# Kernel optimization log

Hardware: AMD Instinct MI355X
Metric: run time of the kernel (lower is better)

## Reference

```python
import jax, jax.numpy as jnp
import numpy as np
import math

B, T, D = 4, 2048, 1024
N, D_OUT = 1024, 1024
EPS_A = 1e-4
PROJ_BOUND = 1.0


def setup_inputs() -> dict:
    key = jax.random.key(0)
    ks = jax.random.split(key, 4)
    # reset_parameters: rho=0.99, delta0=1.0
    rho, delta0 = 0.99, 1.0
    alpha0 = -math.log(rho) / delta0
    alpha_log_val = math.log(math.expm1(alpha0))
    delta_bias_val = math.log(math.expm1(delta0))
    return {
        "u": jax.random.normal(ks[0], (B, T, D), dtype=jnp.float32),
        "z0": jnp.zeros((B, N), dtype=jnp.float32),
        "W_in_raw": 0.02 * jax.random.normal(ks[1], (N, D), dtype=jnp.float32),
        "W_out_raw": 0.02 * jax.random.normal(ks[2], (D_OUT, N), dtype=jnp.float32),
        "pn_w": 0.02 * jax.random.normal(ks[3], (3 * N, D), dtype=jnp.float32),
        "pn_b": jnp.zeros((3 * N,), dtype=jnp.float32),
        "alpha_log": jnp.full((N,), alpha_log_val, dtype=jnp.float32),
        "delta_bias": jnp.full((N,), delta_bias_val, dtype=jnp.float32),
        "log_gamma": jnp.float32(0.0),
    }


def _bounded_linear(x, W, bound):
    # y = x @ (W/scale)^T with ||W/scale||_2 <= bound (exact spectral norm)
    sigma = jnp.maximum(jnp.linalg.norm(W, ord=2), 1e-5)
    scale = jnp.maximum(sigma / bound, 1.0)
    return x @ (W / scale).T


def reference(u, z0, W_in_raw, W_out_raw, pn_w, pn_b, alpha_log, delta_bias, log_gamma):
    g = jnp.exp(log_gamma)
    u_scaled = g * _bounded_linear(u, W_in_raw, PROJ_BOUND)        # (B,T,N)
    raw = u @ pn_w.T + pn_b                                        # (B,T,3N)
    delta_raw, b_raw, c_raw = jnp.split(raw, 3, axis=-1)
    delta = jax.nn.softplus(delta_raw + delta_bias)
    alpha = jax.nn.softplus(alpha_log)                             # (N,)
    a = jnp.minimum(jnp.exp(-delta * alpha), 1.0 - EPS_A)          # (B,T,N)
    b = jnp.tanh(b_raw)
    c = jnp.tanh(c_raw)
    # exact spectral norm of [[a,b],[c,0]] per coordinate
    p = a * a + c * c
    r = b * b
    q = a * b
    disc = (p - r) * (p - r) + 4.0 * q * q
    lam_max = 0.5 * (p + r + jnp.sqrt(disc + 1e-12))
    sigma = jnp.sqrt(lam_max + 1e-12)
    scale = jnp.maximum(sigma, 1.0)
    a, b, c = a / scale, b / scale, c / scale
    # diagonal recurrence z_{t+1} = a_t * z_t + b_t * u_scaled_t via associative scan
    bu = b * u_scaled
    bu = bu.at[:, 0].add(a[:, 0] * z0)
    def combine(x, y):
        a1, b1 = x
        a2, b2 = y
        return (a2 * a1, a2 * b1 + b2)
    _, z_next = jax.lax.associative_scan(combine, (a, bu), axis=1)  # z_1..z_T (B,T,N)
    # y_t = W_out (c_t * z_t) with z_t = state BEFORE update (one-step delay)
    states = jnp.concatenate([z0[:, None, :], z_next[:, :-1, :]], axis=1)  # z_0..z_{T-1}
    y_hat = c * states
    y = _bounded_linear(y_hat, W_out_raw, PROJ_BOUND)              # (B,T,D_out)
    return y
```

## Files before the change

kernel.cpp:

```cpp
#include <hip/hip_runtime.h>
#include <stdint.h>

#define B_ 4
#define T_ 2048
#define D_ 1024
#define N_ 1024
#define TC 16
#define NCH (T_/TC)
#define SQN 6

typedef __attribute__((ext_vector_type(4))) float f32x4;
typedef __attribute__((ext_vector_type(8))) short bf16x8;
typedef __attribute__((ext_vector_type(4))) unsigned short us4;

__device__ __forceinline__ unsigned short f2bf(float f){
  unsigned int u = __float_as_uint(f);
  return (unsigned short)((u + 0x7fffu + ((u >> 16) & 1u)) >> 16);
}
__device__ __forceinline__ float bf2f(unsigned short h){
  return __uint_as_float(((unsigned int)h) << 16);
}

__device__ __forceinline__ float inv_scale(const float* __restrict__ sc, int z){
  float ll = 0.f, w = 1.f, t = 1.f;
  #pragma unroll
  for (int i = 0; i <= SQN; i++){
    t = sc[8 + 2*i + z];
    ll += w * __logf(t);
    w *= 0.5f;
  }
  float F = sc[8 + 2*(SQN+1) + z];
  ll += w * __logf(F / (t*t));
  float sig = fmaxf(__expf(0.5f * ll), 1e-5f);
  return 1.f / fmaxf(sig, 1.f);
}

#define U4    2097152
#define WIN4   262144
#define PNW4   786432
#define WOUT4  262144
#define CONV_BLOCKS ((U4 + WIN4 + PNW4 + WOUT4 + 255)/256)

__global__ void k_convert_all(const float* __restrict__ u, const float* __restrict__ Win,
                              const float* __restrict__ pnw, const float* __restrict__ Wout,
                              unsigned short* __restrict__ u16, unsigned short* __restrict__ Wcat16,
                              unsigned short* __restrict__ Wout16, float* __restrict__ sc){
  if (blockIdx.x == 0 && threadIdx.x < 64) sc[threadIdx.x] = 0.f;
  long i = (long)blockIdx.x * 256 + threadIdx.x;
  const float* src; unsigned short* dst; long o;
  if (i < U4)                      { src = u;    dst = u16;               o = i; }
  else if (i < U4+WIN4)            { src = Win;  dst = Wcat16;            o = i - U4; }
  else if (i < U4+WIN4+PNW4)       { src = pnw;  dst = Wcat16 + 1048576;  o = i - (U4+WIN4); }
  else if (i < U4+WIN4+PNW4+WOUT4) { src = Wout; dst = Wout16;            o = i - (U4+WIN4+PNW4); }
  else return;
  float4 v = ((const float4*)src)[o];
  us4 w;
  w.x = f2bf(v.x); w.y = f2bf(v.y); w.z = f2bf(v.z); w.w = f2bf(v.w);
  ((us4*)dst)[o] = w;
}

__device__ __forceinline__ void load_lds16(const unsigned short* g, unsigned short* l){
  __builtin_amdgcn_global_load_lds((const __attribute__((address_space(1))) void*)g,
                                   (__attribute__((address_space(3))) void*)l, 16, 0, 0);
}

template<int OUTBF16>
__global__ __launch_bounds__(256) void k_gemm(
    const unsigned short* __restrict__ A,
    const unsigned short* __restrict__ Bmat,
    void* __restrict__ C0,
    int M, int N, int K,
    const float* __restrict__ sc, int step)
{
  __shared__ alignas(16) unsigned short As[128*64];
  __shared__ alignas(16) unsigned short Bs[128*64];
  const int tid = threadIdx.x;
  const int wid = tid >> 6;
  const int lane = tid & 63;
  const int bn = blockIdx.x, bm = blockIdx.y;

  char* C = (char*)C0;
  float outscale = (step >= 0) ? inv_scale(sc, step) : 1.f;

  const int wr = wid >> 1, wc = wid & 1;
  const int rg = lane >> 3;
  const int cby = (lane & 7) << 4;
  const int srow0 = wid * 32;
  const int frow = lane & 15;
  const int kgrp = lane >> 4;

  const size_t Abase = (size_t)bm * 128 * K;
  const size_t Bbase = (size_t)bn * 128 * K;

  f32x4 acc[4][4] = {};

  for (int kt = 0; kt < K; kt += 64){
    #pragma unroll
    for (int i = 0; i < 4; i++){
      int r = srow0 + i*8 + rg;
      int cb = cby ^ ((r & 7) << 4);
      load_lds16(A    + Abase + (size_t)r*K + kt + (cb >> 1), As + (srow0 + i*8)*64);
      load_lds16(Bmat + Bbase + (size_t)r*K + kt + (cb >> 1), Bs + (srow0 + i*8)*64);
    }
    __syncthreads();
    #pragma unroll
    for (int kk = 0; kk < 2; kk++){
      const int kbyte = kk*64 + kgrp*16;
      bf16x8 af[4], bfv[4];
      #pragma unroll
      for (int m = 0; m < 4; m++){
        int r = wr*64 + m*16 + frow;
        af[m] = *(const bf16x8*)((const char*)As + r*128 + (kbyte ^ ((r & 7) << 4)));
      }
      #pragma unroll
      for (int n2 = 0; n2 < 4; n2++){
        int r = wc*64 + n2*16 + frow;
        bfv[n2] = *(const bf16x8*)((const char*)Bs + r*128 + (kbyte ^ ((r & 7) << 4)));
      }
      #pragma unroll
      for (int m = 0; m < 4; m++)
        #pragma unroll
        for (int n2 = 0; n2 < 4; n2++)
          acc[m][n2] = __builtin_amdgcn_mfma_f32_16x16x32_bf16(af[m], bfv[n2], acc[m][n2], 0, 0, 0);
    }
    __syncthreads();
  }

  const int row0 = bm*128 + wr*64;
  const int col0 = bn*128 + wc*64 + frow;
  #pragma unroll
  for (int m = 0; m < 4; m++){
    #pragma unroll
    for (int n2 = 0; n2 < 4; n2++){
      const int col = col0 + n2*16;
      const int rb = row0 + m*16 + kgrp*4;
      #pragma unroll
      for (int j = 0; j < 4; j++){
        float v = acc[m][n2][j] * outscale;
        if (OUTBF16) ((unsigned short*)C)[(size_t)(rb + j)*N + col] = f2bf(v);
        else         ((float*)C)[(size_t)(rb + j)*N + col] = v;
      }
    }
  }
}

__global__ __launch_bounds__(256) void k_sq(
    const unsigned short* __restrict__ A0, unsigned short* __restrict__ C0,
    const unsigned short* __restrict__ A1, unsigned short* __restrict__ C1,
    float* __restrict__ sc, int step)
{
  __shared__ alignas(16) unsigned short As0[64*128], Bs0[64*128];
  __shared__ alignas(16) unsigned short As1[64*128], Bs1[64*128];
  const int tid = threadIdx.x;
  const int wid = tid >> 6;
  const int lane = tid & 63;
  const int z = blockIdx.z;

  int x = blockIdx.x, bm = 0;
  while (x >= 16 - bm){ x -= 16 - bm; bm++; }
  const int bn = bm + x;

  const unsigned short* A = z ? A1 : A0;
  unsigned short* C = z ? C1 : C0;
  float outscale = 1.f;
  if (step > 0){ float t = sc[8 + (step-1)*2 + z]; outscale = 1.f/(t*t); }

  const int wr = wid >> 1, wc = wid & 1;
  const int frow = lane & 15;
  const int kgrp = lane >> 4;

  const int srl = lane >> 4;
  const int sgr = lane & 15;
  const int swzr = wid*4 + srl;
  const int scol_e = ((sgr ^ swzr) << 3);

  const size_t Arow = (size_t)bm * 64;
  const size_t Brow = (size_t)bn * 64;

  f32x4 acc[2][2] = {};

  auto stage = [&](unsigned short* as, unsigned short* bs, int t){
    const int kt = t * 128;
    #pragma unroll
    for (int i = 0; i < 4; i++){
      int r = i*16 + wid*4 + srl;
      load_lds16(A + (Arow + r)*1024 + kt + scol_e, as + (i*16 + wid*4)*128);
      load_lds16(A + (Brow + r)*1024 + kt + scol_e, bs + (i*16 + wid*4)*128);
    }
  };

  auto compute = [&](const unsigned short* as, const unsigned short* bs){
    #pragma unroll
    for (int ks = 0; ks < 4; ks++){
      const int kb = ks*64 + kgrp*16;
      bf16x8 af[2], bfv[2];
      #pragma unroll
      for (int m = 0; m < 2; m++){
        int r = wr*32 + m*16 + frow;
        af[m] = *(const bf16x8*)((const char*)as + r*256 + (kb ^ (frow << 4)));
      }
      #pragma unroll
      for (int n2 = 0; n2 < 2; n2++){
        int r = wc*32 + n2*16 + frow;
        bfv[n2] = *(const bf16x8*)((const char*)bs + r*256 + (kb ^ (frow << 4)));
      }
      #pragma unroll
      for (int m = 0; m < 2; m++)
        #pragma unroll
        for (int n2 = 0; n2 < 2; n2++)
          acc[m][n2] = __builtin_amdgcn_mfma_f32_16x16x32_bf16(af[m], bfv[n2], acc[m][n2], 0, 0, 0);
    }
  };

  stage(As0, Bs0, 0);
  __syncthreads();
  for (int t2 = 0; t2 < 8; t2 += 2){
    if (t2 + 1 < 8) stage(As1, Bs1, t2 + 1);
    compute(As0, Bs0);
    __syncthreads();
    if (t2 + 2 < 8) stage(As0, Bs0, t2 + 2);
    compute(As1, Bs1);
    __syncthreads();
  }

  const int row0 = bm*64 + wr*32;
  const int col0 = bn*64 + wc*32 + frow;
  float fr = 0.f;
  #pragma unroll
  for (int m = 0; m < 2; m++){
    #pragma unroll
    for (int n2 = 0; n2 < 2; n2++){
      const int col = col0 + n2*16;
      const int rb = row0 + m*16 + kgrp*4;
      us4 tw;
      #pragma unroll
      for (int j = 0; j < 4; j++){
        float v = acc[m][n2][j] * outscale;
        unsigned short h = f2bf(v);
        C[(size_t)(rb + j)*1024 + col] = h;
        tw[j] = h;
        fr += v*v;
      }
      if (bm != bn)
        *(us4*)(C + (size_t)col*1024 + rb) = tw;
    }
  }
  if (bm == bn && wr == wc){
    int j = frow - kgrp*4;
    if (j >= 0 && j < 4){
      float d = (acc[0][0][j] + acc[1][1][j]) * outscale;
      atomicAdd(&sc[8 + step*2 + z], d);
    }
  }
  if (step == SQN){
    if (bm != bn) fr *= 2.f;
    #pragma unroll
    for (int off = 32; off; off >>= 1) fr += __shfl_down(fr, off, 64);
    if (lane == 0) atomicAdd(&sc[8 + 2*(SQN+1) + z], fr);
  }
}

__device__ __forceinline__ float softplusf(float x){
  return (x > 0.f) ? (x + __logf(1.f + __expf(-x))) : __logf(1.f + __expf(x));
}
__device__ __forceinline__ float tanhfastf(float x){
  float e = __expf(2.f * x);
  return 1.f - 2.f/(e + 1.f);
}
__device__ __forceinline__ void abc_from(float pin, float draw, float braw, float craw,
    float alpha, float ginv, float& a_o, float& bu_o, float& c_o){
  float sp = softplusf(draw);
  float av = __expf(-sp * alpha);
  av = fminf(av, 1.f - 1e-4f);
  float bv = tanhfastf(braw);
  float cv = tanhfastf(craw);
  float p = av*av + cv*cv;
  float r = bv*bv;
  float q = av*bv;
  float pr = p - r;
  float disc = pr*pr + 4.f*q*q;
  float lam = 0.5f*(p + r + sqrtf(disc + 1e-12f));
  float sig = sqrtf(lam + 1e-12f);
  float inv = 1.f / fmaxf(sig, 1.f);
  a_o = av * inv;
  c_o = cv * inv;
  bu_o = (bv * inv) * (pin * ginv);
}

__global__ __launch_bounds__(256) void k_pass1(
    const unsigned short* __restrict__ P,
    const float* __restrict__ alog, const float* __restrict__ dbias,
    const float* __restrict__ pnb, const float* __restrict__ lgam,
    const float* __restrict__ sc,
    float* __restrict__ Asum, float* __restrict__ Ssum)
{
  const int tid = threadIdx.x;
  const int n0 = tid*4;
  const int ch = blockIdx.x, b = blockIdx.y;
  const float ginv = __expf(lgam[0]) * inv_scale(sc, 0);
  float alpha[4], bd[4], bb[4], bc[4], A[4], S[4];
  #pragma unroll
  for (int j = 0; j < 4; j++){
    alpha[j] = softplusf(alog[n0+j]);
    bd[j] = dbias[n0+j] + pnb[n0+j];
    bb[j] = pnb[N_ + n0+j];
    bc[j] = pnb[2*N_ + n0+j];
    A[j] = 1.f; S[j] = 0.f;
  }
  const unsigned short* Pr = P + (size_t)(b*T_ + ch*TC) * (4*N_);
  #pragma unroll 2
  for (int i = 0; i < TC; i++){
    us4 vp = *(const us4*)(Pr + n0);
    us4 vd = *(const us4*)(Pr + N_ + n0);
    us4 vb = *(const us4*)(Pr + 2*N_ + n0);
    us4 vc = *(const us4*)(Pr + 3*N_ + n0);
    #pragma unroll
    for (int j = 0; j < 4; j++){
      float a, bu, c;
      abc_from(bf2f(vp[j]), bf2f(vd[j]) + bd[j], bf2f(vb[j]) + bb[j], bf2f(vc[j]) + bc[j],
               alpha[j], ginv, a, bu, c);
      S[j] = fmaf(a, S[j], bu);
      A[j] *= a;
    }
    Pr += 4*N_;
  }
  const size_t idx = (size_t)(b*NCH + ch)*N_ + n0;
  #pragma unroll
  for (int j = 0; j < 4; j++){ Asum[idx+j] = A[j]; Ssum[idx+j] = S[j]; }
}

__global__ void k_pass2(const float* __restrict__ Asum, const float* __restrict__ Ssum,
                        const float* __restrict__ z0, float* __restrict__ Zent)
{
  const int n = blockIdx.x*256 + threadIdx.x;
  const int b = blockIdx.y;
  float z = z0[b*N_ + n];
  for (int ch = 0; ch < NCH; ch++){
    const size_t idx = (size_t)(b*NCH + ch)*N_ + n;
    Zent[idx] = z;
    z = fmaf(Asum[idx], z, Ssum[idx]);
  }
}

__global__ __launch_bounds__(256) void k_pass3(
    const unsigned short* __restrict__ P,
    const float* __restrict__ alog, const float* __restrict__ dbias,
    const float* __restrict__ pnb, const float* __restrict__ lgam,
    const float* __restrict__ sc, const float* __restrict__ Zent,
    unsigned short* __restrict__ yh)
{
  const int tid = threadIdx.x;
  const int n0 = tid*4;
  const int ch = blockIdx.x, b = blockIdx.y;
  const float ginv = __expf(lgam[0]) * inv_scale(sc, 0);
  float alpha[4], bd[4], bb[4], bc[4], z[4];
  #pragma unroll
  for (int j = 0; j < 4; j++){
    alpha[j] = softplusf(alog[n0+j]);
    bd[j] = dbias[n0+j] + pnb[n0+j];
    bb[j] = pnb[N_ + n0+j];
    bc[j] = pnb[2*N_ + n0+j];
  }
  const size_t zidx = (size_t)(b*NCH + ch)*N_ + n0;
  #pragma unroll
  for (int j = 0; j < 4; j++) z[j] = Zent[zidx+j];
  const unsigned short* Pr = P + (size_t)(b*T_ + ch*TC) * (4*N_);
  unsigned short* Y = yh + (size_t)(b*T_ + ch*TC)*N_ + n0;
  #pragma unroll 2
  for (int i = 0; i < TC; i++){
    us4 vp = *(const us4*)(Pr + n0);
    us4 vd = *(const us4*)(Pr + N_ + n0);
    us4 vb = *(const us4*)(Pr + 2*N_ + n0);
    us4 vc = *(const us4*)(Pr + 3*N_ + n0);
    us4 ow;
    #pragma unroll
    for (int j = 0; j < 4; j++){
      float a, bu, c;
      abc_from(bf2f(vp[j]), bf2f(vd[j]) + bd[j], bf2f(vb[j]) + bb[j], bf2f(vc[j]) + bc[j],
               alpha[j], ginv, a, bu, c);
      float yv = c * z[j];
      z[j] = fmaf(a, z[j], bu);
      ow[j] = f2bf(yv);
    }
    *(us4*)Y = ow;
    Y += N_;
    Pr += 4*N_;
  }
}

extern "C" void kernel_launch(void* const* d_in, const int* in_sizes, int n_in,
                              void* d_out, int out_size, void* d_ws, size_t ws_size,
                              hipStream_t stream)
{
  const float* u    = (const float*)d_in[0];
  const float* z0   = (const float*)d_in[1];
  const float* Win  = (const float*)d_in[2];
  const float* Wout = (const float*)d_in[3];
  const float* pnw  = (const float*)d_in[4];
  const float* pnb  = (const float*)d_in[5];
  const float* alog = (const float*)d_in[6];
  const float* dbias= (const float*)d_in[7];
  const float* lgam = (const float*)d_in[8];

  char* ws = (char*)d_ws;
  size_t off = 0;
  auto alloc = [&](size_t bytes) -> void* {
    void* p = ws + off;
    off += (bytes + 255) & ~(size_t)255;
    return p;
  };
  float*          sc     = (float*)         alloc(1024);
  unsigned short* u16    = (unsigned short*)alloc((size_t)8192*1024*2);
  unsigned short* Wcat16 = (unsigned short*)alloc((size_t)4096*1024*2);
  unsigned short* Wout16 = (unsigned short*)alloc((size_t)1024*1024*2);
  unsigned short* P16    = (unsigned short*)alloc((size_t)8192*4096*2);
  unsigned short* yh16   = (unsigned short*)alloc((size_t)8192*1024*2);
  unsigned short* Hping  = (unsigned short*)alloc((size_t)2*1024*1024*2);
  unsigned short* Hpong  = (unsigned short*)alloc((size_t)2*1024*1024*2);
  float*          Asum   = (float*)alloc((size_t)B_*NCH*N_*4);
  float*          Ssum   = (float*)alloc((size_t)B_*NCH*N_*4);
  float*          Zent   = (float*)alloc((size_t)B_*NCH*N_*4);

  k_convert_all<<<CONV_BLOCKS, 256, 0, stream>>>(u, Win, pnw, Wout, u16, Wcat16, Wout16, sc);

  dim3 gsq(136, 1, 2);
  k_sq<<<gsq, 256, 0, stream>>>(Wcat16, Hping, Wout16, Hping + (size_t)1024*1024, sc, 0);
  unsigned short* hin = Hping;
  unsigned short* hout = Hpong;
  for (int s = 1; s <= SQN; s++){
    k_sq<<<gsq, 256, 0, stream>>>(hin, hout, hin + (size_t)1024*1024, hout + (size_t)1024*1024, sc, s);
    unsigned short* t = hin; hin = hout; hout = t;
  }

  dim3 g1(4096/128, 8192/128);
  k_gemm<1><<<g1, 256, 0, stream>>>(u16, Wcat16, P16, 8192, 4096, 1024, sc, -1);

  dim3 gp1(NCH, B_);
  k_pass1<<<gp1, 256, 0, stream>>>(P16, alog, dbias, pnb, lgam, sc, Asum, Ssum);
  dim3 gp2(N_/256, B_);
  k_pass2<<<gp2, 256, 0, stream>>>(Asum, Ssum, z0, Zent);
  k_pass3<<<gp1, 256, 0, stream>>>(P16, alog, dbias, pnb, lgam, sc, Zent, yh16);

  dim3 g2(1024/128, 8192/128);
  k_gemm<0><<<g2, 256, 0, stream>>>(yh16, Wout16, d_out, 8192, 1024, 1024, sc, 1);
}
```

Baseline: 300.2 us.

## Interleave projection weight rows so scan kernels read contiguous per-channel quadruples

The concatenated W_in/pn_w weight is written in interleaved row order (u_scaled, delta, b, c for each channel adjacent), so the GEMM output places the four values for a channel contiguously and the scan kernels load two 16-byte vectors instead of four strided 8-byte ones. The power-iteration squaring kernel takes a 4096 row stride for the interleaved matrix at step 0 to read the W_in rows. The GEMM precomputes global and LDS address pointers and offsets outside the k loop, and the per-coordinate scale uses rsqrt with a min instead of sqrt plus a divide. This couples the weight layout across convert, spectral-norm and scan kernels, so any missed index would silently corrupt results.

```diff
diff --git a/kernel.cpp b/kernel.cpp
--- a/kernel.cpp
+++ b/kernel.cpp
@@ -47,16 +47,25 @@
                               unsigned short* __restrict__ Wout16, float* __restrict__ sc){
   if (blockIdx.x == 0 && threadIdx.x < 64) sc[threadIdx.x] = 0.f;
   long i = (long)blockIdx.x * 256 + threadIdx.x;
-  const float* src; unsigned short* dst; long o;
-  if (i < U4)                      { src = u;    dst = u16;               o = i; }
-  else if (i < U4+WIN4)            { src = Win;  dst = Wcat16;            o = i - U4; }
-  else if (i < U4+WIN4+PNW4)       { src = pnw;  dst = Wcat16 + 1048576;  o = i - (U4+WIN4); }
-  else if (i < U4+WIN4+PNW4+WOUT4) { src = Wout; dst = Wout16;            o = i - (U4+WIN4+PNW4); }
-  else return;
+  const float* src; long o; size_t didx; unsigned short* dbuf;
+  if (i < U4){
+    src = u; o = i; dbuf = u16; didx = (size_t)o;
+  } else if (i < U4+WIN4){
+    o = i - U4; src = Win;
+    int n = (int)(o >> 8), c4 = (int)(o & 255);
+    dbuf = Wcat16; didx = (size_t)(4*n)*256 + c4;
+  } else if (i < U4+WIN4+PNW4){
+    o = i - (U4+WIN4); src = pnw;
+    int m = (int)(o >> 8), c4 = (int)(o & 255);
+    int s = (m >> 10) + 1, n = m & 1023;
+    dbuf = Wcat16; didx = (size_t)(4*n + s)*256 + c4;
+  } else if (i < U4+WIN4+PNW4+WOUT4){
+    o = i - (U4+WIN4+PNW4); src = Wout; dbuf = Wout16; didx = (size_t)o;
+  } else return;
   float4 v = ((const float4*)src)[o];
   us4 w;
   w.x = f2bf(v.x); w.y = f2bf(v.y); w.z = f2bf(v.z); w.w = f2bf(v.w);
-  ((us4*)dst)[o] = w;
+  ((us4*)dbuf)[didx] = w;
 }
 
 __device__ __forceinline__ void load_lds16(const unsigned short* g, unsigned short* l){
@@ -89,34 +98,55 @@
   const int frow = lane & 15;
   const int kgrp = lane >> 4;
 
-  const size_t Abase = (size_t)bm * 128 * K;
-  const size_t Bbase = (size_t)bn * 128 * K;
+  const unsigned short* ap[4];
+  const unsigned short* bp[4];
+  unsigned short* adst[4];
+  unsigned short* bdst[4];
+  #pragma unroll
+  for (int i = 0; i < 4; i++){
+    int r = srow0 + i*8 + rg;
+    int cb = cby ^ ((r & 7) << 4);
+    ap[i] = A    + (size_t)(bm*128 + r)*K + (cb >> 1);
+    bp[i] = Bmat + (size_t)(bn*128 + r)*K + (cb >> 1);
+    adst[i] = As + (srow0 + i*8)*64;
+    bdst[i] = Bs + (srow0 + i*8)*64;
+  }
+
+  int aoff[4][2], boff[4][2];
+  #pragma unroll
+  for (int m = 0; m < 4; m++){
+    int r = wr*64 + m*16 + frow;
+    #pragma unroll
+    for (int kk = 0; kk < 2; kk++)
+      aoff[m][kk] = r*128 + ((kk*64 + kgrp*16) ^ ((r & 7) << 4));
+  }
+  #pragma unroll
+  for (int n2 = 0; n2 < 4; n2++){
+    int r = wc*64 + n2*16 + frow;
+    #pragma unroll
+    for (int kk = 0; kk < 2; kk++)
+      boff[n2][kk] = r*128 + ((kk*64 + kgrp*16) ^ ((r & 7) << 4));
+  }
 
   f32x4 acc[4][4] = {};
 
   for (int kt = 0; kt < K; kt += 64){
     #pragma unroll
     for (int i = 0; i < 4; i++){
-      int r = srow0 + i*8 + rg;
-      int cb = cby ^ ((r & 7) << 4);
-      load_lds16(A    + Abase + (size_t)r*K + kt + (cb >> 1), As + (srow0 + i*8)*64);
-      load_lds16(Bmat + Bbase + (size_t)r*K + kt + (cb >> 1), Bs + (srow0 + i*8)*64);
+      load_lds16(ap[i], adst[i]);
+      load_lds16(bp[i], bdst[i]);
+      ap[i] += 64; bp[i] += 64;
     }
     __syncthreads();
     #pragma unroll
     for (int kk = 0; kk < 2; kk++){
-      const int kbyte = kk*64 + kgrp*16;
       bf16x8 af[4], bfv[4];
       #pragma unroll
-      for (int m = 0; m < 4; m++){
-        int r = wr*64 + m*16 + frow;
-        af[m] = *(const bf16x8*)((const char*)As + r*128 + (kbyte ^ ((r & 7) << 4)));
-      }
-      #pragma unroll
-      for (int n2 = 0; n2 < 4; n2++){
-        int r = wc*64 + n2*16 + frow;
-        bfv[n2] = *(const bf16x8*)((const char*)Bs + r*128 + (kbyte ^ ((r & 7) << 4)));
-      }
+      for (int m = 0; m < 4; m++)
+        af[m] = *(const bf16x8*)((const char*)As + aoff[m][kk]);
+      #pragma unroll
+      for (int n2 = 0; n2 < 4; n2++)
+        bfv[n2] = *(const bf16x8*)((const char*)Bs + boff[n2][kk]);
       #pragma unroll
       for (int m = 0; m < 4; m++)
         #pragma unroll
@@ -162,6 +192,7 @@
 
   const unsigned short* A = z ? A1 : A0;
   unsigned short* C = z ? C1 : C0;
+  const size_t rs = (step == 0 && z == 0) ? 4096 : 1024;
   float outscale = 1.f;
   if (step > 0){ float t = sc[8 + (step-1)*2 + z]; outscale = 1.f/(t*t); }
 
@@ -184,8 +215,8 @@
     #pragma unroll
     for (int i = 0; i < 4; i++){
       int r = i*16 + wid*4 + srl;
-      load_lds16(A + (Arow + r)*1024 + kt + scol_e, as + (i*16 + wid*4)*128);
-      load_lds16(A + (Brow + r)*1024 + kt + scol_e, bs + (i*16 + wid*4)*128);
+      load_lds16(A + (Arow + r)*rs + kt + scol_e, as + (i*16 + wid*4)*128);
+      load_lds16(A + (Brow + r)*rs + kt + scol_e, bs + (i*16 + wid*4)*128);
     }
   };
 
@@ -280,8 +311,7 @@
   float pr = p - r;
   float disc = pr*pr + 4.f*q*q;
   float lam = 0.5f*(p + r + sqrtf(disc + 1e-12f));
-  float sig = sqrtf(lam + 1e-12f);
-  float inv = 1.f / fmaxf(sig, 1.f);
+  float inv = fminf(rsqrtf(lam + 1e-12f), 1.f);
   a_o = av * inv;
   c_o = cv * inv;
   bu_o = (bv * inv) * (pin * ginv);
@@ -307,22 +337,23 @@
     bc[j] = pnb[2*N_ + n0+j];
     A[j] = 1.f; S[j] = 0.f;
   }
-  const unsigned short* Pr = P + (size_t)(b*T_ + ch*TC) * (4*N_);
+  const unsigned short* Pr = P + (size_t)(b*T_ + ch*TC) * 4096 + 4*n0;
   #pragma unroll 2
   for (int i = 0; i < TC; i++){
-    us4 vp = *(const us4*)(Pr + n0);
-    us4 vd = *(const us4*)(Pr + N_ + n0);
-    us4 vb = *(const us4*)(Pr + 2*N_ + n0);
-    us4 vc = *(const us4*)(Pr + 3*N_ + n0);
+    bf16x8 e0 = *(const bf16x8*)Pr;
+    bf16x8 e1 = *(const bf16x8*)(Pr + 8);
     #pragma unroll
     for (int j = 0; j < 4; j++){
+      const bf16x8& e = (j < 2) ? e0 : e1;
+      const int o = (j & 1)*4;
       float a, bu, c;
-      abc_from(bf2f(vp[j]), bf2f(vd[j]) + bd[j], bf2f(vb[j]) + bb[j], bf2f(vc[j]) + bc[j],
+      abc_from(bf2f((unsigned short)e[o]),   bf2f((unsigned short)e[o+1]) + bd[j],
+               bf2f((unsigned short)e[o+2]) + bb[j], bf2f((unsigned short)e[o+3]) + bc[j],
                alpha[j], ginv, a, bu, c);
       S[j] = fmaf(a, S[j], bu);
       A[j] *= a;
     }
-    Pr += 4*N_;
+    Pr += 4096;
   }
   const size_t idx = (size_t)(b*NCH + ch)*N_ + n0;
   #pragma unroll
@@ -364,19 +395,20 @@
   const size_t zidx = (size_t)(b*NCH + ch)*N_ + n0;
   #pragma unroll
   for (int j = 0; j < 4; j++) z[j] = Zent[zidx+j];
-  const unsigned short* Pr = P + (size_t)(b*T_ + ch*TC) * (4*N_);
+  const unsigned short* Pr = P + (size_t)(b*T_ + ch*TC) * 4096 + 4*n0;
   unsigned short* Y = yh + (size_t)(b*T_ + ch*TC)*N_ + n0;
   #pragma unroll 2
   for (int i = 0; i < TC; i++){
-    us4 vp = *(const us4*)(Pr + n0);
-    us4 vd = *(const us4*)(Pr + N_ + n0);
-    us4 vb = *(const us4*)(Pr + 2*N_ + n0);
-    us4 vc = *(const us4*)(Pr + 3*N_ + n0);
+    bf16x8 e0 = *(const bf16x8*)Pr;
+    bf16x8 e1 = *(const bf16x8*)(Pr + 8);
     us4 ow;
     #pragma unroll
     for (int j = 0; j < 4; j++){
+      const bf16x8& e = (j < 2) ? e0 : e1;
+      const int o = (j & 1)*4;
       float a, bu, c;
-      abc_from(bf2f(vp[j]), bf2f(vd[j]) + bd[j], bf2f(vb[j]) + bb[j], bf2f(vc[j]) + bc[j],
+      abc_from(bf2f((unsigned short)e[o]),   bf2f((unsigned short)e[o+1]) + bd[j],
+               bf2f((unsigned short)e[o+2]) + bb[j], bf2f((unsigned short)e[o+3]) + bc[j],
                alpha[j], ginv, a, bu, c);
       float yv = c * z[j];
       z[j] = fmaf(a, z[j], bu);
@@ -384,7 +416,7 @@
     }
     *(us4*)Y = ow;
     Y += N_;
-    Pr += 4*N_;
+    Pr += 4096;
   }
 }
 
```

Result: faster. 290.6 us (-3.2%).
